# Kernel tuning notes

Measured on AMD Instinct MI355X. Metric: run time of the kernel, lower is better.

Reference implementation:

```python
import jax, jax.numpy as jnp
import numpy as np

A = -0.75  # torch bicubic cubic-convolution coefficient

def _cubic_k(t):
    at = jnp.abs(t)
    return jnp.where(at <= 1, (A + 2) * at**3 - (A + 3) * at**2 + 1,
           jnp.where(at < 2, A * at**3 - 5 * A * at**2 + 8 * A * at - 4 * A, 0.0))

def _resize_last(x, out_size):
    # bicubic, align_corners=True, along last axis
    in_size = x.shape[-1]
    pos = jnp.arange(out_size, dtype=x.dtype) * ((in_size - 1) / (out_size - 1))
    i0 = jnp.floor(pos).astype(jnp.int32)
    frac = pos - i0
    offs = jnp.arange(-1, 3, dtype=jnp.int32)                    # 4 taps
    idx = jnp.clip(i0[None] + offs[:, None], 0, in_size - 1)     # [4, out]
    w = _cubic_k(frac[None] - offs[:, None].astype(x.dtype))     # [4, out]
    g = x[..., idx]                                              # [..., 4, out]
    return jnp.einsum('...ko,ko->...o', g, w)

def bicubic(x, H, W):
    x = _resize_last(x, W)
    x = jnp.swapaxes(_resize_last(jnp.swapaxes(x, -1, -2), H), -1, -2)
    return x

def conv(x, w, b):
    y = jax.lax.conv_general_dilated(x, w, (1, 1), 'SAME',
                                     dimension_numbers=('NCHW', 'OIHW', 'NCHW'))
    return y + b[None, :, None, None]

def pool(x):
    return jax.lax.reduce_window(x, -jnp.inf, jax.lax.max, (1, 1, 2, 2), (1, 1, 2, 2), 'VALID')

def extract(x, ws, bs):
    # feat1: vgg19 features[:2]
    x1 = jax.nn.relu(conv(x, ws[0], bs[0]))
    # feat2: vgg19 features[2:18]
    h = jax.nn.relu(conv(x1, ws[1], bs[1])); h = pool(h)
    h = jax.nn.relu(conv(h, ws[2], bs[2]))
    h = jax.nn.relu(conv(h, ws[3], bs[3])); h = pool(h)
    for i in range(4, 8):
        h = jax.nn.relu(conv(h, ws[i], bs[i]))
    h = bicubic(h, x1.shape[-2], x1.shape[-1])
    return jnp.concatenate([x1, h], axis=1)  # [B, 320, H, W]

def normalizer(f1, f2):
    B, C = f1.shape[:2]
    a = f1.reshape(B, C, -1)
    b = f2.reshape(B, C, -1)
    xc = jnp.concatenate([a, b], axis=-1)
    mean = xc.mean(-1, keepdims=True)
    std = xc.mean(-1, keepdims=True)  # faithful to original source bug: std = mean
    a = (a - mean) / (std + 1e-8)
    b = (b - mean) / (std + 1e-8)
    return a.reshape(f1.shape), b.reshape(f2.shape)

_CHANS = [(3, 64), (64, 64), (64, 128), (128, 128), (128, 256), (256, 256), (256, 256), (256, 256)]

def setup_inputs() -> dict:
    key = jax.random.key(0)
    ks = jax.random.split(key, 20)
    inp = {}
    for i, (ci, co) in enumerate(_CHANS):
        inp[f'w{i}'] = jax.random.normal(ks[i], (co, ci, 3, 3), jnp.float32) * np.sqrt(2.0 / (ci * 9))
        inp[f'b{i}'] = jnp.zeros((co,), jnp.float32)
    inp['x_ref'] = jax.random.normal(ks[16], (2, 3, 96, 96), jnp.float32)
    inp['x_template'] = jax.random.normal(ks[17], (2, 3, 48, 48), jnp.float32)
    inp['coef_ref'] = jnp.float32(1.0)
    inp['coef_tmp'] = jnp.float32(1.0)
    return inp

def reference(x_ref, x_template, coef_ref, coef_tmp,
              w0, b0, w1, b1, w2, b2, w3, b3, w4, b4, w5, b5, w6, b6, w7, b7):
    ws = [w0, w1, w2, w3, w4, w5, w6, w7]
    bs = [b0, b1, b2, b3, b4, b5, b6, b7]
    fref = extract(x_ref, ws, bs)
    ftem = extract(x_template, ws, bs)
    fref, ftem = normalizer(fref, ftem)
    B, C, m, n = fref.shape
    _, _, p, q = ftem.shape
    dist = jnp.einsum('bcmn,bcpq->bmnpq', fref, ftem).reshape(B, m * n, p * q)
    conf_ref = jax.nn.softmax(coef_ref * dist, axis=-2)
    conf_tmp = jax.nn.softmax(coef_tmp * dist, axis=-1)
    confidence = jnp.sqrt(conf_ref * conf_tmp)
    vals, _ = jax.lax.top_k(confidence, 10)
    values = vals.mean(-1, keepdims=True).reshape(B, m, n, 1)
    return values
```

## Files before the change

### kernel.cpp

```cpp
#include <hip/hip_runtime.h>
#include <math.h>

#define CK_A (-0.75f)

typedef __attribute__((ext_vector_type(8))) short bf16x8;
typedef __attribute__((ext_vector_type(4))) float f32x4;

struct CImg { const float* in; float* out; int H, W, tiles; long inBS, outBS, sStride; };

__device__ __forceinline__ float cubicw(float t){
  float at = fabsf(t);
  float at2 = at*at, at3 = at2*at;
  if (at <= 1.f) return (CK_A+2.f)*at3 - (CK_A+3.f)*at2 + 1.f;
  if (at < 2.f)  return CK_A*at3 - 5.f*CK_A*at2 + 8.f*CK_A*at - 4.f*CK_A;
  return 0.f;
}

__device__ __forceinline__ unsigned short f2bf_rne(float f){
  unsigned int u = __float_as_uint(f);
  unsigned int r = (u + 0x7fffu + ((u>>16)&1u)) >> 16;
  return (unsigned short)r;
}
__device__ __forceinline__ float bf2f(unsigned short h){
  return __uint_as_float(((unsigned int)h)<<16);
}

__device__ __forceinline__ void merge_ms(float& m, float& s, float m2, float s2){
  float M = fmaxf(m, m2);
  s = s*__expf(m - M) + s2*__expf(m2 - M);
  m = M;
}

#define MFB(a,b,c) __builtin_amdgcn_mfma_f32_16x16x32_bf16(a,b,c,0,0,0)

__global__ __launch_bounds__(256) void conv0_d(CImg A, CImg B,
    const float* __restrict__ w, const float* __restrict__ bias){
  bool isA = (int)blockIdx.x < A.tiles;
  const float* in = isA ? A.in : B.in;
  float* out = isA ? A.out : B.out;
  int H = isA ? A.H : B.H, W = isA ? A.W : B.W;
  long inBS = isA ? A.inBS : B.inBS, outBS = isA ? A.outBS : B.outBS;
  int tile = isA ? blockIdx.x : blockIdx.x - A.tiles;
  int tilesX = (W + 15) >> 4;
  int tx0 = (tile % tilesX) << 4, ty0 = (tile / tilesX) << 4;
  int cob = blockIdx.y * 4;
  int b = blockIdx.z;
  int lx = threadIdx.x & 15, ly = threadIdx.x >> 4;
  __shared__ float tile_s[3][18][20];
  float acc[4] = {0.f,0.f,0.f,0.f};
  const float* inb = in + (long)b*inBS;
  int ox = tx0+lx, oy = ty0+ly;

  for (int idx = threadIdx.x; idx < 3*324; idx += 256){
    int cl = idx/324, rem = idx - cl*324;
    int r = rem/18, c = rem - r*18;
    int gy = ty0 + r - 1, gx = tx0 + c - 1;
    const float* ic = inb + (long)cl*H*W;
    tile_s[cl][r][c] = (gy>=0 && gy<H && gx>=0 && gx<W) ? ic[(long)gy*W+gx] : 0.f;
  }
  __syncthreads();
  #pragma unroll
  for (int cl=0; cl<3; cl++){
    float t00=tile_s[cl][ly+0][lx+0], t01=tile_s[cl][ly+0][lx+1], t02=tile_s[cl][ly+0][lx+2];
    float t10=tile_s[cl][ly+1][lx+0], t11=tile_s[cl][ly+1][lx+1], t12=tile_s[cl][ly+1][lx+2];
    float t20=tile_s[cl][ly+2][lx+0], t21=tile_s[cl][ly+2][lx+1], t22=tile_s[cl][ly+2][lx+2];
    #pragma unroll
    for (int j=0;j<4;j++){
      const float* wp = w + ((long)(cob+j)*3 + cl)*9;
      float a = acc[j];
      a = fmaf(t00, wp[0], a); a = fmaf(t01, wp[1], a); a = fmaf(t02, wp[2], a);
      a = fmaf(t10, wp[3], a); a = fmaf(t11, wp[4], a); a = fmaf(t12, wp[5], a);
      a = fmaf(t20, wp[6], a); a = fmaf(t21, wp[7], a); a = fmaf(t22, wp[8], a);
      acc[j] = a;
    }
  }
  if (ox < W && oy < H){
    #pragma unroll
    for (int j=0;j<4;j++){
      float v = fmaxf(acc[j] + bias[cob+j], 0.f);
      out[(long)b*outBS + (long)(cob+j)*H*W + (long)oy*W + ox] = v;
    }
  }
}

__global__ void prep_w_all(const float* __restrict__ w1, const float* __restrict__ w2,
                           const float* __restrict__ w3, const float* __restrict__ w4,
                           const float* __restrict__ w5, const float* __restrict__ w6,
                           const float* __restrict__ w7, unsigned short* __restrict__ wp){
  const int ciT[7] = {64,64,128,128,256,256,256};
  const int coT[7] = {64,128,128,256,256,256,256};
  int l = blockIdx.y;
  const float* w = l==0?w1: l==1?w2: l==2?w3: l==3?w4: l==4?w5: l==5?w6: w7;
  long offv = 0;
  for (int i=0;i<7;i++){ if (i<l) offv += 9L*ciT[i]*coT[i]*2; }
  long total = 9L*ciT[l]*coT[l]*2;
  long e = (long)blockIdx.x*256 + threadIdx.x;
  if (e >= total) return;
  int CI = ciT[l], CO = coT[l];
  int j = (int)(e & 7);
  int lane = (int)((e>>3) & 63);
  int h = (int)((e>>9) & 1);
  long rem = e >> 10;
  int G = CO >> 4, KC = CI >> 5;
  int g = (int)(rem % G); long q = rem / G;
  int kc = (int)(q % KC); int o = (int)(q / KC);
  int co = (g<<4) + (lane & 15);
  int ci = (kc<<5) + ((lane>>4)<<3) + j;
  float v = w[((long)co*CI + ci)*9 + o];
  unsigned short hi = f2bf_rne(v);
  wp[offv + e] = (h==0) ? hi : f2bf_rne(v - bf2f(hi));
}

union AB { bf16x8 v; uint4 u; };

__global__ __launch_bounds__(256) void conv_mfma_d(
    CImg A, CImg B, const unsigned short* __restrict__ Wp,
    const float* __restrict__ bias, int CI, int CO, int nci, int S)
{
  bool isA = (int)blockIdx.x < A.tiles;
  const float* in = isA ? A.in : B.in;
  float* out = isA ? A.out : B.out;
  int H = isA ? A.H : B.H, W = isA ? A.W : B.W;
  long inBS = isA ? A.inBS : B.inBS, outBS = isA ? A.outBS : B.outBS;
  long sStride = isA ? A.sStride : B.sStride;
  int tile = isA ? blockIdx.x : blockIdx.x - A.tiles;

  int HW = H*W;
  int tilesX = (W+7)>>3;
  int tx0 = (tile % tilesX)<<3, ty0 = (tile / tilesX)<<3;
  int cobase = blockIdx.y << 6;
  int s = blockIdx.z % S, b = blockIdx.z / S;
  int tid = threadIdx.x, lane = tid & 63, wid = tid>>6;
  int wm = wid>>1, wn = wid&1;
  int KC = CI>>5, G = CO>>4;
  __shared__ __align__(16) unsigned short Bth[4000];
  __shared__ __align__(16) unsigned short Btl[4000];
  const float* inb = in + (long)b*inBS;

  int sofs[13]; int sla[13];
  #pragma unroll
  for (int i=0;i<13;i++){
    int e = tid + i*256;
    int cidx = e / 100, pix = e - cidx*100;
    int hy = pix/10, hx = pix - hy*10;
    int gy = ty0 - 1 + hy, gx = tx0 - 1 + hx;
    bool v = (gy>=0) && (gy<H) && (gx>=0) && (gx<W);
    sofs[i] = v ? (cidx*HW + gy*W + gx) : -1;
    sla[i] = pix*40 + cidx;
  }

  int n15 = lane & 15;
  int klane8 = (lane>>4)<<3;
  int p0 = wn*32 + n15;
  int base0 = ((p0>>3)*10 + (p0&7))*40 + klane8;
  int p1 = p0 + 16;
  int base1 = ((p1>>3)*10 + (p1&7))*40 + klane8;
  int g0 = (cobase>>4) + wm*2;

  f32x4 acc[2][2];
  #pragma unroll
  for (int i=0;i<2;i++)
    #pragma unroll
    for (int j=0;j<2;j++) acc[i][j] = (f32x4){0.f,0.f,0.f,0.f};

  int nkc = nci >> 5;
  for (int kk=0; kk<nkc; kk++){
    int ci0 = s*nci + (kk<<5);
    __syncthreads();
    #pragma unroll
    for (int i=0;i<12;i++){
      float v = (sofs[i] >= 0) ? inb[(long)ci0*HW + sofs[i]] : 0.f;
      unsigned short h = f2bf_rne(v);
      Bth[sla[i]] = h;
      Btl[sla[i]] = f2bf_rne(v - bf2f(h));
    }
    if (tid < 128){
      float v = (sofs[12] >= 0) ? inb[(long)ci0*HW + sofs[12]] : 0.f;
      unsigned short h = f2bf_rne(v);
      Bth[sla[12]] = h;
      Btl[sla[12]] = f2bf_rne(v - bf2f(h));
    }
    __syncthreads();
    int kc = ci0 >> 5;
    const unsigned short* wpb = Wp + (long)kc*G*1024 + (long)lane*8;
    #pragma unroll
    for (int o=0;o<9;o++){
      const int dy = o/3, dx = o - dy*3;
      const int sh = (dy*10+dx)*40;
      const unsigned short* wo = wpb + (long)o*KC*G*1024;
      AB a0h,a0l,a1h,a1l, b0h,b0l,b1h,b1l;
      a0h.u = *(const uint4*)(wo + (long)g0*1024);
      a0l.u = *(const uint4*)(wo + (long)g0*1024 + 512);
      a1h.u = *(const uint4*)(wo + (long)(g0+1)*1024);
      a1l.u = *(const uint4*)(wo + (long)(g0+1)*1024 + 512);
      b0h.v = *(const bf16x8*)&Bth[base0 + sh];
      b0l.v = *(const bf16x8*)&Btl[base0 + sh];
      b1h.v = *(const bf16x8*)&Bth[base1 + sh];
      b1l.v = *(const bf16x8*)&Btl[base1 + sh];
      acc[0][0] = MFB(a0h.v, b0l.v, acc[0][0]);
      acc[0][0] = MFB(a0l.v, b0h.v, acc[0][0]);
      acc[0][0] = MFB(a0h.v, b0h.v, acc[0][0]);
      acc[0][1] = MFB(a0h.v, b1l.v, acc[0][1]);
      acc[0][1] = MFB(a0l.v, b1h.v, acc[0][1]);
      acc[0][1] = MFB(a0h.v, b1h.v, acc[0][1]);
      acc[1][0] = MFB(a1h.v, b0l.v, acc[1][0]);
      acc[1][0] = MFB(a1l.v, b0h.v, acc[1][0]);
      acc[1][0] = MFB(a1h.v, b0h.v, acc[1][0]);
      acc[1][1] = MFB(a1h.v, b1l.v, acc[1][1]);
      acc[1][1] = MFB(a1l.v, b1h.v, acc[1][1]);
      acc[1][1] = MFB(a1h.v, b1h.v, acc[1][1]);
    }
  }

  float* outp = out + (long)s*sStride + (long)b*outBS;
  #pragma unroll
  for (int ng=0; ng<2; ng++){
    int p = wn*32 + ng*16 + n15;
    int gy = ty0 + (p>>3), gx = tx0 + (p&7);
    bool ok = (gy<H) && (gx<W);
    #pragma unroll
    for (int mg=0; mg<2; mg++){
      #pragma unroll
      for (int r=0;r<4;r++){
        if (ok){
          int co = cobase + wm*32 + mg*16 + ((lane>>4)<<2) + r;
          float v = acc[mg][ng][r];
          if (bias) v = fmaxf(v + bias[co], 0.f);
          outp[(long)co*HW + (long)gy*W + gx] = v;
        }
      }
    }
  }
}

__global__ void reduce_d(const float* __restrict__ pA, const float* __restrict__ pB,
                         const float* __restrict__ bias,
                         float* __restrict__ oA, float* __restrict__ oB,
                         int S, long sStrA, long sStrB, int CO, int HWa, int HWb,
                         long oBSa, long oBSb){
  int img = blockIdx.y;
  const float* part = img ? pB : pA;
  float* out = img ? oB : oA;
  int HW = img ? HWb : HWa;
  long sStride = img ? sStrB : sStrA;
  long outBS = img ? oBSb : oBSa;
  long tot = 2L*CO*HW;
  long e = (long)blockIdx.x*256 + threadIdx.x;
  if (e >= tot) return;
  long b = e / ((long)CO*HW);
  long r = e - b*(long)CO*HW;
  float v = 0.f;
  for (int s=0;s<S;s++) v += part[(long)s*sStride + e];
  int co = (int)(r / HW);
  out[b*outBS + r] = fmaxf(v + bias[co], 0.f);
}

__global__ void maxpool2_d(const float* __restrict__ inA, float* __restrict__ outA, long NCa, int HiA, int WiA,
                           const float* __restrict__ inB, float* __restrict__ outB, long NCb, int HiB, int WiB){
  const float* in = blockIdx.y ? inB : inA;
  float* out = blockIdx.y ? outB : outA;
  long NC = blockIdx.y ? NCb : NCa;
  int Hi = blockIdx.y ? HiB : HiA, Wi = blockIdx.y ? WiB : WiA;
  int Ho = Hi>>1, Wo = Wi>>1;
  long total = NC * Ho * Wo;
  long idx = (long)blockIdx.x*256 + threadIdx.x;
  if (idx >= total) return;
  int x = (int)(idx % Wo); long t = idx / Wo; int y = (int)(t % Ho); long nc = t / Ho;
  const float* p = in + (nc*Hi + 2*y)*(long)Wi + 2*x;
  out[idx] = fmaxf(fmaxf(p[0], p[1]), fmaxf(p[Wi], p[Wi+1]));
}

__global__ __launch_bounds__(256) void bicubic_d(
    const float* __restrict__ inA, float* __restrict__ outA,
    const float* __restrict__ inB, float* __restrict__ outB){
  int c = blockIdx.x;
  int img = blockIdx.y >> 1, b = blockIdx.y & 1;
  const float* in = img ? inB : inA;
  float* out = img ? outB : outA;
  int Hin = img ? 12 : 24, Win = Hin, Hout = img ? 48 : 96, Wout = Hout;
  long inBS = img ? 256L*144 : 256L*576;
  long outBS = img ? 320L*2304 : 320L*9216;
  __shared__ float s[576];
  const float* ip = in + (long)b*inBS + (long)c*Hin*Win;
  float* op = out + (long)b*outBS + (long)c*Hout*Wout;
  int n = Hin*Win;
  for (int i = threadIdx.x; i < n; i += 256) s[i] = ip[i];
  __syncthreads();
  float scy = (float)((double)(Hin-1)/(double)(Hout-1));
  float scx = scy;
  int total = Hout*Wout;
  for (int idx = threadIdx.x; idx < total; idx += 256){
    int ox = idx % Wout, oy = idx / Wout;
    float py = oy * scy, px = ox * scx;
    float iy0f = floorf(py), ix0f = floorf(px);
    int iy0 = (int)iy0f, ix0 = (int)ix0f;
    float fy = py - iy0f, fx = px - ix0f;
    float wy[4], wx[4]; int xs[4], ys[4];
    #pragma unroll
    for (int t=0;t<4;t++){
      wy[t] = cubicw(fy - (float)(t-1));
      wx[t] = cubicw(fx - (float)(t-1));
      ys[t] = min(max(iy0 + t - 1, 0), Hin-1);
      xs[t] = min(max(ix0 + t - 1, 0), Win-1);
    }
    float acc = 0.f;
    #pragma unroll
    for (int i=0;i<4;i++){
      const float* row = &s[ys[i]*Win];
      float rs = wx[0]*row[xs[0]] + wx[1]*row[xs[1]] + wx[2]*row[xs[2]] + wx[3]*row[xs[3]];
      acc = fmaf(wy[i], rs, acc);
    }
    op[idx] = acc;
  }
}

__global__ __launch_bounds__(256) void mean_k(const float* __restrict__ fR, const float* __restrict__ fT, float* __restrict__ mean){
  int c = blockIdx.x % 320, b = blockIdx.x / 320;
  const float* a = fR + ((long)b*320+c)*9216L;
  const float* t = fT + ((long)b*320+c)*2304L;
  float s = 0.f;
  for (int i=threadIdx.x;i<9216;i+=256) s += a[i];
  for (int i=threadIdx.x;i<2304;i+=256) s += t[i];
  __shared__ float sm[4];
  for (int o=32;o;o>>=1) s += __shfl_down(s,o);
  int lane = threadIdx.x & 63, wv = threadIdx.x >> 6;
  if (lane==0) sm[wv] = s;
  __syncthreads();
  if (threadIdx.x==0) mean[b*320+c] = (sm[0]+sm[1]+sm[2]+sm[3]) * (1.f/11520.f);
}

__global__ __launch_bounds__(256) void split_bf16_d(const float* __restrict__ fR, const float* __restrict__ fT,
    const float* __restrict__ mean,
    unsigned short* __restrict__ AhR, unsigned short* __restrict__ AlR,
    unsigned short* __restrict__ BhT, unsigned short* __restrict__ BlT){
  bool isR = blockIdx.x < 288;
  const float* feat = isR ? fR : fT;
  unsigned short* oh = isR ? AhR : BhT;
  unsigned short* ol = isR ? AlR : BlT;
  int P = isR ? 9216 : 2304;
  int m0 = (isR ? blockIdx.x : blockIdx.x - 288) * 32;
  int b = blockIdx.y;
  __shared__ unsigned int t[32][321];
  int ml = threadIdx.x & 31, kq = threadIdx.x >> 5;
  const float* fp = feat + (long)b*320*P + m0 + ml;
  for (int k = kq*40; k < kq*40+40; k++){
    float mu = mean[b*320+k];
    float v = (fp[(long)k*P] - mu) / (mu + 1e-8f);
    unsigned short h = f2bf_rne(v);
    unsigned short l = f2bf_rne(v - bf2f(h));
    t[ml][k] = ((unsigned int)h<<16) | l;
  }
  __syncthreads();
  long base = ((long)b*P + m0)*320;
  for (int idx = threadIdx.x; idx < 32*320; idx += 256){
    int m = idx/320, k = idx - m*320;
    unsigned int p = t[m][k];
    oh[base + (long)m*320 + k] = (unsigned short)(p>>16);
    ol[base + (long)m*320 + k] = (unsigned short)(p & 0xffffu);
  }
}

__global__ __launch_bounds__(256) void gemm_mfma(
    const unsigned short* __restrict__ Ah, const unsigned short* __restrict__ Al,
    const unsigned short* __restrict__ Bh, const unsigned short* __restrict__ Bl,
    float* __restrict__ D, const float* __restrict__ coefr,
    float* __restrict__ pm, float* __restrict__ ps){
  const int N = 2304, K = 320;
  int n0 = blockIdx.x*128, m0 = blockIdx.y*128;
  __shared__ __align__(16) unsigned short Bs[2][128][72];
  int tid = threadIdx.x, lane = tid & 63, wid = tid >> 6;
  int wm = wid >> 1, wn = wid & 1;
  int n15 = lane & 15, q8 = (lane>>4)<<3;
  f32x4 acc[4][4];
  #pragma unroll
  for (int i=0;i<4;i++)
    #pragma unroll
    for (int j=0;j<4;j++) acc[i][j] = (f32x4){0.f,0.f,0.f,0.f};

  const unsigned short* aRowH[4];
  const unsigned short* aRowL[4];
  #pragma unroll
  for (int g=0; g<4; g++){
    long row = m0 + wm*64 + g*16 + n15;
    aRowH[g] = Ah + row*K + q8;
    aRowL[g] = Al + row*K + q8;
  }

  for (int k0=0; k0<K; k0+=64){
    __syncthreads();
    #pragma unroll
    for (int i=0;i<8;i++){
      int e = i*256 + tid;
      int tsr = e >> 10;
      int rem = e & 1023;
      int row = rem >> 3, seg = rem & 7;
      const unsigned short* src = tsr ? Bl : Bh;
      uint4 v = *(const uint4*)(src + (long)(n0+row)*K + k0 + seg*8);
      *(uint4*)&Bs[tsr][row][seg*8] = v;
    }
    __syncthreads();

    #pragma unroll
    for (int kk=0; kk<2; kk++){
      int ko = k0 + kk*32;
      AB af[2][4], bf[2][4];
      #pragma unroll
      for (int g=0; g<4; g++){
        af[0][g].u = *(const uint4*)(aRowH[g] + ko);
        af[1][g].u = *(const uint4*)(aRowL[g] + ko);
        bf[0][g].v = *(const bf16x8*)&Bs[0][wn*64 + g*16 + n15][kk*32 + q8];
        bf[1][g].v = *(const bf16x8*)&Bs[1][wn*64 + g*16 + n15][kk*32 + q8];
      }
      #pragma unroll
      for (int mg=0; mg<4; mg++)
        #pragma unroll
        for (int ng=0; ng<4; ng++){
          acc[mg][ng] = MFB(af[0][mg].v, bf[1][ng].v, acc[mg][ng]);
          acc[mg][ng] = MFB(af[1][mg].v, bf[0][ng].v, acc[mg][ng]);
          acc[mg][ng] = MFB(af[0][mg].v, bf[0][ng].v, acc[mg][ng]);
        }
    }
  }
  __syncthreads();

  #pragma unroll
  for (int mg=0; mg<4; mg++)
    #pragma unroll
    for (int ng=0; ng<4; ng++){
      int col = n0 + wn*64 + ng*16 + n15;
      #pragma unroll
      for (int r=0;r<4;r++){
        int rowv = m0 + wm*64 + mg*16 + (lane>>4)*4 + r;
        D[(long)rowv*N + col] = acc[mg][ng][r];
      }
    }

  float cr = *coefr;
  float* red = (float*)&Bs[0][0][0];
  float pmv[4], psv[4];
  #pragma unroll
  for (int ng=0; ng<4; ng++){
    float m = -INFINITY;
    #pragma unroll
    for (int mg=0; mg<4; mg++)
      #pragma unroll
      for (int r=0;r<4;r++) m = fmaxf(m, cr*acc[mg][ng][r]);
    float s = 0.f;
    #pragma unroll
    for (int mg=0; mg<4; mg++)
      #pragma unroll
      for (int r=0;r<4;r++) s += __expf(cr*acc[mg][ng][r] - m);
    #pragma unroll
    for (int o=16;o<64;o<<=1){
      float m2 = __shfl_xor(m,o), s2 = __shfl_xor(s,o);
      merge_ms(m,s,m2,s2);
    }
    pmv[ng]=m; psv[ng]=s;
  }
  if ((lane>>4)==0){
    #pragma unroll
    for (int ng=0; ng<4; ng++){
      int cl = wn*64 + ng*16 + lane;
      red[wm*128 + cl] = pmv[ng];
      red[256 + wm*128 + cl] = psv[ng];
    }
  }
  __syncthreads();
  if (wm==0 && (lane>>4)==0){
    #pragma unroll
    for (int ng=0; ng<4; ng++){
      int cl = wn*64 + ng*16 + lane;
      float m = pmv[ng], s = psv[ng];
      merge_ms(m, s, red[128+cl], red[384+cl]);
      pm[(long)blockIdx.y*2304 + n0 + cl] = m;
      ps[(long)blockIdx.y*2304 + n0 + cl] = s;
    }
  }
}

__global__ void colstat_merge(const float* __restrict__ pm, const float* __restrict__ ps,
                              float* __restrict__ qcol){
  int idx = blockIdx.x*256 + threadIdx.x;
  if (idx >= 2304) return;
  float m=-INFINITY, s=0.f;
  for (int k=0;k<72;k++) merge_ms(m, s, pm[(long)k*2304+idx], ps[(long)k*2304+idx]);
  qcol[idx] = 0.5f*m + 0.5f*__logf(s);
}

__global__ __launch_bounds__(256) void conf_topk_f(const float* __restrict__ D,
    const float* __restrict__ coefr, const float* __restrict__ coeft,
    const float* __restrict__ qcol, float* __restrict__ outp){
  int m = blockIdx.x;
  const float* drow = D + (long)m*2304;
  int tid = threadIdx.x, lane = tid & 63, wv = tid >> 6;
  float ct = *coeft, cr = *coefr;
  float v[9], tv[9];
  #pragma unroll
  for (int i=0;i<9;i++){ v[i] = drow[tid + i*256]; tv[i] = ct * v[i]; }

  __shared__ float sred[8];
  __shared__ unsigned int cand[40];

  float mx = tv[0];
  #pragma unroll
  for (int i=1;i<9;i++) mx = fmaxf(mx, tv[i]);
  #pragma unroll
  for (int o=1;o<64;o<<=1) mx = fmaxf(mx, __shfl_xor(mx, o));
  if (lane==0) sred[wv] = mx;
  __syncthreads();
  mx = fmaxf(fmaxf(sred[0],sred[1]), fmaxf(sred[2],sred[3]));
  float s = 0.f;
  #pragma unroll
  for (int i=0;i<9;i++) s += __expf(tv[i]-mx);
  #pragma unroll
  for (int o=1;o<64;o<<=1) s += __shfl_xor(s, o);
  if (lane==0) sred[4+wv] = s;
  __syncthreads();
  float rs = sred[4]+sred[5]+sred[6]+sred[7];
  float rho = 0.5f*mx + 0.5f*__logf(rs);
  float hc = 0.5f*(cr+ct);

  unsigned int key[9];
  #pragma unroll
  for (int i=0;i<9;i++){
    int n = i*256 + tid;
    float t = fmaf(hc, v[i], -qcol[n]);
    unsigned int b = __float_as_uint(t);
    b ^= (b >> 31) ? 0xFFFFFFFFu : 0x80000000u;
    key[i] = (b & 0xFFFFF000u) | (unsigned)n;
  }

  for (int t10=0; t10<10; t10++){
    unsigned int lb = key[0];
    #pragma unroll
    for (int i=1;i<9;i++) lb = lb > key[i] ? lb : key[i];
    unsigned int wb = lb;
    #pragma unroll
    for (int o=1;o<64;o<<=1){
      unsigned int x = (unsigned int)__shfl_xor((int)wb, o);
      wb = wb > x ? wb : x;
    }
    if (lane==0) cand[wv*10 + t10] = wb;
    #pragma unroll
    for (int i=0;i<9;i++) if (key[i]==wb) key[i]=0;
  }
  __syncthreads();

  if (wv == 0){
    unsigned int k = (lane < 40) ? cand[lane] : 0u;
    int sel = -1;
    for (int t10=0; t10<10; t10++){
      unsigned int wb = k;
      #pragma unroll
      for (int o=1;o<64;o<<=1){
        unsigned int x = (unsigned int)__shfl_xor((int)wb, o);
        wb = wb > x ? wb : x;
      }
      if (k == wb) k = 0;
      if (lane == t10) sel = (int)(wb & 0xFFFu);
    }
    float c = 0.f;
    if (sel >= 0){
      float t = fmaf(hc, drow[sel], -qcol[sel]);
      c = __expf(t - rho);
    }
    #pragma unroll
    for (int o=1;o<64;o<<=1) c += __shfl_xor(c, o);
    if (lane == 0) outp[m] = c * 0.1f;
  }
}

extern "C" void kernel_launch(void* const* d_in, const int* in_sizes, int n_in,
                              void* d_out, int out_size, void* d_ws, size_t ws_size,
                              hipStream_t stream) {
  const float *W[8], *Bp[8], *xr, *xt, *cr, *ct;
  if (in_sizes[0] == 1728){
    for (int i=0;i<8;i++){ W[i]=(const float*)d_in[2*i]; Bp[i]=(const float*)d_in[2*i+1]; }
    xr=(const float*)d_in[16]; xt=(const float*)d_in[17];
    cr=(const float*)d_in[18]; ct=(const float*)d_in[19];
  } else {
    xr=(const float*)d_in[0]; xt=(const float*)d_in[1];
    cr=(const float*)d_in[2]; ct=(const float*)d_in[3];
    for (int i=0;i<8;i++){ W[i]=(const float*)d_in[4+2*i]; Bp[i]=(const float*)d_in[5+2*i]; }
  }

  const int convCI[8] = {3,64,64,128,128,256,256,256};
  const int convCO[8] = {64,64,128,128,256,256,256,256};
  long wpoff[8]; long wtot = 0;
  for (int l=1;l<8;l++){ wpoff[l] = wtot; wtot += 9L*convCI[l]*convCO[l]*2; }

  float* ws = (float*)d_ws;
  long off = 0;
  auto alloc = [&](long nfl){ float* p = ws + off; off += (nfl + 63) & ~63L; return p; };
  float* featR = alloc(2L*320*9216);
  float* featT = alloc(2L*320*2304);
  float* meanb = alloc(640);
  float* pm    = alloc(72L*2304);
  float* ps    = alloc(72L*2304);
  float* qcol  = alloc(2304);
  unsigned short* wp = (unsigned short*)alloc((wtot+1)/2);
  float* scratch = alloc(9216L*2304);
  if ((size_t)(off*4) > ws_size) return;

  unsigned short* AhR = (unsigned short*)alloc((2L*9216*320 + 1)/2);
  unsigned short* AlR = (unsigned short*)alloc((2L*9216*320 + 1)/2);
  unsigned short* BhT = (unsigned short*)alloc((2L*2304*320 + 1)/2);
  unsigned short* BlT = (unsigned short*)alloc((2L*2304*320 + 1)/2);
  if ((size_t)(off*4) > ws_size) return;

  float* rA = scratch;
  float* rB = rA + 1179648;
  float* rC = rB + 294912;
  float* rD = rC + 589824;
  float* rE = rD + 589824;
  float* rF = rE + 147456;
  float* rG = rF + 294912;
  float* a2 = rG + 294912;
  float* b2 = a2 + 294912;
  float* c2 = b2 + 73728;
  float* d2 = c2 + 147456;
  float* e2 = d2 + 147456;
  float* f2 = e2 + 36864;
  float* g2 = f2 + 73728;
  float* tPR = g2 + 73728;
  float* tPT = tPR + 1179648;
  float* dist = scratch;

  auto mkimg = [](const float* in, float* out, int H, int Wd, int tiles,
                  long inBS, long outBS, long sStr){
    CImg c; c.in=in; c.out=out; c.H=H; c.W=Wd; c.tiles=tiles;
    c.inBS=inBS; c.outBS=outBS; c.sStride=sStr; return c;
  };

  prep_w_all<<<dim3(4608,7), 256, 0, stream>>>(W[1],W[2],W[3],W[4],W[5],W[6],W[7], wp);

  {
    CImg A = mkimg(xr, featR, 96,96, 36, 3L*9216, 320L*9216, 0);
    CImg B = mkimg(xt, featT, 48,48, 9, 3L*2304, 320L*2304, 0);
    conv0_d<<<dim3(45,16,2), 256, 0, stream>>>(A, B, W[0], Bp[0]);
  }
  {
    CImg A = mkimg(featR, rA, 96,96, 144, 320L*9216, 64L*9216, 0);
    CImg B = mkimg(featT, a2, 48,48, 36, 320L*2304, 64L*2304, 0);
    conv_mfma_d<<<dim3(180,1,2), 256, 0, stream>>>(A,B, wp+wpoff[1], Bp[1], 64,64,64,1);
  }
  maxpool2_d<<<dim3(1152,2), 256, 0, stream>>>(rA,rB,128,96,96, a2,b2,128,48,48);
  {
    CImg A = mkimg(rB, tPR, 48,48, 36, 64L*2304, 128L*2304, 589824);
    CImg B = mkimg(b2, tPT, 24,24, 9, 64L*576, 128L*576, 147456);
    conv_mfma_d<<<dim3(45,2,4), 256, 0, stream>>>(A,B, wp+wpoff[2], nullptr, 64,128,32,2);
    reduce_d<<<dim3(2304,2), 256, 0, stream>>>(tPR,tPT,Bp[2], rC,c2, 2, 589824,147456, 128, 2304,576, 128L*2304, 128L*576);
  }
  {
    CImg A = mkimg(rC, tPR, 48,48, 36, 128L*2304, 128L*2304, 589824);
    CImg B = mkimg(c2, tPT, 24,24, 9, 128L*576, 128L*576, 147456);
    conv_mfma_d<<<dim3(45,2,4), 256, 0, stream>>>(A,B, wp+wpoff[3], nullptr, 128,128,64,2);
    reduce_d<<<dim3(2304,2), 256, 0, stream>>>(tPR,tPT,Bp[3], rD,d2, 2, 589824,147456, 128, 2304,576, 128L*2304, 128L*576);
  }
  maxpool2_d<<<dim3(576,2), 256, 0, stream>>>(rD,rE,256,48,48, d2,e2,256,24,24);
  {
    CImg A = mkimg(rE, tPR, 24,24, 9, 128L*576, 256L*576, 294912);
    CImg B = mkimg(e2, tPT, 12,12, 4, 128L*144, 256L*144, 73728);
    conv_mfma_d<<<dim3(13,4,8), 256, 0, stream>>>(A,B, wp+wpoff[4], nullptr, 128,256,32,4);
    reduce_d<<<dim3(1152,2), 256, 0, stream>>>(tPR,tPT,Bp[4], rF,f2, 4, 294912,73728, 256, 576,144, 256L*576, 256L*144);
  }
  const float* inR[3] = {rF, rG, rF};  float* outR[3] = {rG, rF, rG};
  const float* inT[3] = {f2, g2, f2};  float* outT[3] = {g2, f2, g2};
  for (int i=0;i<3;i++){
    int l = 5+i;
    CImg A = mkimg(inR[i], tPR, 24,24, 9, 256L*576, 256L*576, 294912);
    CImg B = mkimg(inT[i], tPT, 12,12, 4, 256L*144, 256L*144, 73728);
    conv_mfma_d<<<dim3(13,4,8), 256, 0, stream>>>(A,B, wp+wpoff[l], nullptr, 256,256,64,4);
    reduce_d<<<dim3(1152,2), 256, 0, stream>>>(tPR,tPT,Bp[l], outR[i],outT[i], 4, 294912,73728, 256, 576,144, 256L*576, 256L*144);
  }
  bicubic_d<<<dim3(256,4), 256, 0, stream>>>(rG, featR + 64L*9216, g2, featT + 64L*2304);

  mean_k<<<640, 256, 0, stream>>>(featR, featT, meanb);
  split_bf16_d<<<dim3(360,2), 256, 0, stream>>>(featR, featT, meanb, AhR, AlR, BhT, BlT);

  for (int b=0; b<2; b++){
    gemm_mfma<<<dim3(18,72), 256, 0, stream>>>(
        AhR + (long)b*9216*320, AlR + (long)b*9216*320,
        BhT + (long)b*2304*320, BlT + (long)b*2304*320, dist, cr, pm, ps);
    colstat_merge<<<dim3(9), 256, 0, stream>>>(pm, ps, qcol);
    conf_topk_f<<<dim3(9216), 256, 0, stream>>>(dist, cr, ct, qcol, (float*)d_out + (long)b*9216);
  }
}
```

Before: 505.1 us.

## Stage A and B tiles via direct global-to-LDS loads with XOR swizzle

The similarity GEMM now stages both the A (hi/lo) and B (hi/lo) operand tiles into shared memory with global_load_lds DMA, instead of loading A fragments straight from global memory and copying B through registers. The LDS layout uses an XOR swizzle on 16-byte segments to avoid bank conflicts, and the K step drops from 64 to 32 with a single inner iteration. This removes redundant uncoalesced global reads of A and register round-trips, at the cost of twice as many barrier-separated K iterations with no double buffering.

New measurement: 455.9 us. 1.11x faster.

```diff
diff --git a/kernel.cpp b/kernel.cpp
--- a/kernel.cpp
+++ b/kernel.cpp
@@ -32,6 +32,12 @@
 }
 
 #define MFB(a,b,c) __builtin_amdgcn_mfma_f32_16x16x32_bf16(a,b,c,0,0,0)
+
+typedef const __attribute__((address_space(1))) unsigned int* gp1_t;
+typedef __attribute__((address_space(3))) unsigned int* lp3_t;
+__device__ __forceinline__ void dma16(const void* g, void* l){
+  __builtin_amdgcn_global_load_lds((gp1_t)g, (lp3_t)l, 16, 0, 0);
+}
 
 __global__ __launch_bounds__(256) void conv0_d(CImg A, CImg B,
     const float* __restrict__ w, const float* __restrict__ bias){
@@ -367,59 +373,62 @@
     float* __restrict__ pm, float* __restrict__ ps){
   const int N = 2304, K = 320;
   int n0 = blockIdx.x*128, m0 = blockIdx.y*128;
-  __shared__ __align__(16) unsigned short Bs[2][128][72];
+  __shared__ __align__(16) unsigned short SF[16384];
   int tid = threadIdx.x, lane = tid & 63, wid = tid >> 6;
   int wm = wid >> 1, wn = wid & 1;
-  int n15 = lane & 15, q8 = (lane>>4)<<3;
+  int n15 = lane & 15, q = lane >> 4;
   f32x4 acc[4][4];
   #pragma unroll
   for (int i=0;i<4;i++)
     #pragma unroll
     for (int j=0;j<4;j++) acc[i][j] = (f32x4){0.f,0.f,0.f,0.f};
 
-  const unsigned short* aRowH[4];
-  const unsigned short* aRowL[4];
+  const unsigned short* srcB[8];
+  #pragma unroll
+  for (int i=0;i<8;i++){
+    int li = i*256 + tid;
+    int rem = li & 1023;
+    int row = rem >> 3, sg = rem & 7;
+    int seg = sg ^ (row & 7);
+    if (li < 1024) srcB[i] = ((seg<4) ? Ah : Al) + (long)(m0+row)*K + (seg&3)*8;
+    else           srcB[i] = ((seg<4) ? Bh : Bl) + (long)(n0+row)*K + (seg&3)*8;
+  }
+
+  int aH[4], aL[4], bH[4], bL[4];
   #pragma unroll
   for (int g=0; g<4; g++){
-    long row = m0 + wm*64 + g*16 + n15;
-    aRowH[g] = Ah + row*K + q8;
-    aRowL[g] = Al + row*K + q8;
-  }
-
-  for (int k0=0; k0<K; k0+=64){
+    int ra = wm*64 + g*16 + n15;
+    int rb = wn*64 + g*16 + n15;
+    aH[g] = ra*64 + (( q   ) ^ (ra&7))*8;
+    aL[g] = ra*64 + ((q+4) ^ (ra&7))*8;
+    bH[g] = 8192 + rb*64 + (( q   ) ^ (rb&7))*8;
+    bL[g] = 8192 + rb*64 + ((q+4) ^ (rb&7))*8;
+  }
+
+  for (int k0=0; k0<K; k0+=32){
     __syncthreads();
     #pragma unroll
     for (int i=0;i<8;i++){
-      int e = i*256 + tid;
-      int tsr = e >> 10;
-      int rem = e & 1023;
-      int row = rem >> 3, seg = rem & 7;
-      const unsigned short* src = tsr ? Bl : Bh;
-      uint4 v = *(const uint4*)(src + (long)(n0+row)*K + k0 + seg*8);
-      *(uint4*)&Bs[tsr][row][seg*8] = v;
+      dma16(srcB[i] + k0, (void*)&SF[((i<<8) + (wid<<6))<<3]);
     }
     __syncthreads();
 
-    #pragma unroll
-    for (int kk=0; kk<2; kk++){
-      int ko = k0 + kk*32;
-      AB af[2][4], bf[2][4];
+    AB af[2][4], bf[2][4];
+    #pragma unroll
+    for (int g=0; g<4; g++){
+      af[0][g].v = *(const bf16x8*)&SF[aH[g]];
+      af[1][g].v = *(const bf16x8*)&SF[aL[g]];
+      bf[0][g].v = *(const bf16x8*)&SF[bH[g]];
+      bf[1][g].v = *(const bf16x8*)&SF[bL[g]];
+    }
+    #pragma unroll
+    for (int mg=0; mg<4; mg++)
       #pragma unroll
-      for (int g=0; g<4; g++){
-        af[0][g].u = *(const uint4*)(aRowH[g] + ko);
-        af[1][g].u = *(const uint4*)(aRowL[g] + ko);
-        bf[0][g].v = *(const bf16x8*)&Bs[0][wn*64 + g*16 + n15][kk*32 + q8];
-        bf[1][g].v = *(const bf16x8*)&Bs[1][wn*64 + g*16 + n15][kk*32 + q8];
+      for (int ng=0; ng<4; ng++){
+        acc[mg][ng] = MFB(af[0][mg].v, bf[1][ng].v, acc[mg][ng]);
+        acc[mg][ng] = MFB(af[1][mg].v, bf[0][ng].v, acc[mg][ng]);
+        acc[mg][ng] = MFB(af[0][mg].v, bf[0][ng].v, acc[mg][ng]);
       }
-      #pragma unroll
-      for (int mg=0; mg<4; mg++)
-        #pragma unroll
-        for (int ng=0; ng<4; ng++){
-          acc[mg][ng] = MFB(af[0][mg].v, bf[1][ng].v, acc[mg][ng]);
-          acc[mg][ng] = MFB(af[1][mg].v, bf[0][ng].v, acc[mg][ng]);
-          acc[mg][ng] = MFB(af[0][mg].v, bf[0][ng].v, acc[mg][ng]);
-        }
-    }
   }
   __syncthreads();
 
@@ -430,13 +439,13 @@
       int col = n0 + wn*64 + ng*16 + n15;
       #pragma unroll
       for (int r=0;r<4;r++){
-        int rowv = m0 + wm*64 + mg*16 + (lane>>4)*4 + r;
+        int rowv = m0 + wm*64 + mg*16 + q*4 + r;
         D[(long)rowv*N + col] = acc[mg][ng][r];
       }
     }
 
   float cr = *coefr;
-  float* red = (float*)&Bs[0][0][0];
+  float* red = (float*)&SF[0];
   float pmv[4], psv[4];
   #pragma unroll
   for (int ng=0; ng<4; ng++){
@@ -457,7 +466,7 @@
     }
     pmv[ng]=m; psv[ng]=s;
   }
-  if ((lane>>4)==0){
+  if (q==0){
     #pragma unroll
     for (int ng=0; ng<4; ng++){
       int cl = wn*64 + ng*16 + lane;
@@ -466,7 +475,7 @@
     }
   }
   __syncthreads();
-  if (wm==0 && (lane>>4)==0){
+  if (wm==0 && q==0){
     #pragma unroll
     for (int ng=0; ng<4; ng++){
       int cl = wn*64 + ng*16 + lane;
```
